# Optimization experiments

Measured on AMD Instinct MI355X. Metric: run time of the kernel, lower is better.

The kernel has to match this reference:

```python
import jax, jax.numpy as jnp
import numpy as np

DIM = 128
IND_DIM = 5
HEADS = 4
DIM_HEAD = 32
HIDDEN = HEADS * DIM_HEAD  # 128
SCALE = DIM_HEAD ** -0.5


def setup_inputs() -> dict:
    key = jax.random.key(0)
    ks = jax.random.split(key, 6)
    b, n = 1, 512
    x = jax.random.normal(ks[0], (b, DIM, n), dtype=jnp.float32)
    indicator = jax.random.normal(ks[1], (b, IND_DIM, n, n), dtype=jnp.float32)
    # conv1d kernels with kernel_size=1 are just (out, in) matrices
    w_qkv = jax.random.normal(ks[2], (HIDDEN * 3, DIM), dtype=jnp.float32) * (DIM ** -0.5)
    w_ind = jax.random.normal(ks[3], (HIDDEN * 2, IND_DIM), dtype=jnp.float32) * (IND_DIM ** -0.5)
    w_out = jax.random.normal(ks[4], (DIM, HIDDEN), dtype=jnp.float32) * (HIDDEN ** -0.5)
    b_out = jax.random.normal(ks[5], (DIM,), dtype=jnp.float32) * 0.01
    return {"x": x, "indicator": indicator, "w_qkv": w_qkv,
            "w_ind": w_ind, "w_out": w_out, "b_out": b_out}


def reference(x, indicator, w_qkv, w_ind, w_out, b_out):
    b, c, n = x.shape
    h, dh = HEADS, DIM_HEAD
    # pointwise conv = channel matmul
    qkv = jnp.einsum('oc,bcn->bon', w_qkv, x)  # (b, 3*hidden, n)
    q, k, v = jnp.split(qkv, 3, axis=1)
    q = q.reshape(b, h, dh, n)
    k = k.reshape(b, h, dh, n)
    v = v.reshape(b, h, dh, n)
    ind = jnp.einsum('oc,bcij->boij', w_ind, indicator)  # (b, 2*hidden, n, n)
    ind_q, ind_k = jnp.split(ind, 2, axis=1)
    ind_q = ind_q.reshape(b, h, dh, n, n)
    ind_k = ind_k.reshape(b, h, dh, n, n)
    qq = (q[..., :, None] + ind_q) * SCALE        # (b, h, dh, n, n)
    kk = k[..., None, :] + ind_k                   # (b, h, dh, n, n)
    sim = jnp.einsum('bhdij,bhdij->bhij', qq, kk)  # (b, h, n, n)
    attn = jax.nn.softmax(sim, axis=-1)
    out = jnp.einsum('bhij,bhdj->bhdi', attn, v)   # (b, h, dh, n)
    out = out.reshape(b, h * dh, n)
    return jnp.einsum('oc,bcn->bon', w_out, out) + b_out[None, :, None]
```

## Files before the change

kernel.cpp:

```cpp
#include <hip/hip_runtime.h>
#include <hip/hip_fp16.h>
#include <math.h>

#define N      512
#define DIMC   128
#define HEADS  4
#define DH     32
#define INDC   5
#define SCALE  0.1767766952966369f

#define QKV_ROWS 384
#define AQ_BASE  384
#define AK_BASE  404
#define TOT_ROWS 424
#define NROW_BLK (TOT_ROWS / 4)

#define MHS_F    (TOT_ROWS * N / 2)
#define WOUTT_F  (MHS_F + 64)

__global__ __launch_bounds__(256) void pre_kernel(const float* __restrict__ w_qkv,
                                                  const float* __restrict__ w_ind,
                                                  const float* __restrict__ x,
                                                  const float* __restrict__ w_out,
                                                  float* __restrict__ ws) {
    const int bx = blockIdx.x;
    const int t  = threadIdx.x;
    __half* rows  = (__half*)ws;
    float* MhS    = ws + MHS_F;
    float* w_outT = ws + WOUTT_F;

    if (bx == NROW_BLK) {
        if (blockIdx.y != 0) return;
        __shared__ float mraw[HEADS * INDC * INDC];
        if (t < HEADS * INDC * INDC) {
            const int h = t / 25, c = (t / 5) % 5, cc = t % 5;
            float acc = 0.f;
            for (int d = 0; d < DH; ++d)
                acc = fmaf(w_ind[(h * DH + d) * INDC + c],
                           w_ind[(DIMC + h * DH + d) * INDC + cc], acc);
            mraw[t] = acc;
        }
        __syncthreads();
        if (t < 64) {
            const int h = t >> 4, idx = t & 15;
            const int PC[10]  = {0, 0, 0, 0, 1, 1, 1, 2, 2, 3};
            const int PCC[10] = {1, 2, 3, 4, 2, 3, 4, 3, 4, 4};
            float s = 0.f;
            if (idx < 5) {
                s = mraw[h * 25 + idx * 5 + idx];
            } else if (idx < 15) {
                const int c = PC[idx - 5], cc = PCC[idx - 5];
                s = mraw[h * 25 + c * 5 + cc] + mraw[h * 25 + cc * 5 + c];
            }
            MhS[h * 16 + idx] = s;
        }
        for (int idx = t; idx < DIMC * DIMC; idx += 256) {
            const int o = idx >> 7, c = idx & 127;
            w_outT[c * DIMC + o] = w_out[idx];
        }
        return;
    }

    __shared__ float ws2[4 * DIMC];
    const int o0 = bx * 4;
    for (int idx = t; idx < 4 * DIMC; idx += 256) {
        const int r = idx & 3, m = idx >> 2;
        const int row = o0 + r;
        float val;
        if (row < QKV_ROWS) {
            val = w_qkv[row * DIMC + m];
        } else if (row < AK_BASE) {
            const int rr = row - AQ_BASE, h = rr / INDC, c = rr % INDC;
            float acc = 0.f;
            for (int d = 0; d < DH; ++d)
                acc = fmaf(w_qkv[(h * DH + d) * DIMC + m],
                           w_ind[(DIMC + h * DH + d) * INDC + c], acc);
            val = acc;
        } else {
            const int rr = row - AK_BASE, h = rr / INDC, c = rr % INDC;
            float acc = 0.f;
            for (int d = 0; d < DH; ++d)
                acc = fmaf(w_qkv[(DIMC + h * DH + d) * DIMC + m],
                           w_ind[(h * DH + d) * INDC + c], acc);
            val = acc;
        }
        ws2[m * 4 + r] = val;
    }
    __syncthreads();

    const int i = blockIdx.y * 256 + t;
    float acc[4] = {0.f, 0.f, 0.f, 0.f};
#pragma unroll 8
    for (int c = 0; c < DIMC; ++c) {
        const float xv = x[c * N + i];
        const float4 wv = *(const float4*)(ws2 + c * 4);
        acc[0] = fmaf(wv.x, xv, acc[0]);
        acc[1] = fmaf(wv.y, xv, acc[1]);
        acc[2] = fmaf(wv.z, xv, acc[2]);
        acc[3] = fmaf(wv.w, xv, acc[3]);
    }
#pragma unroll
    for (int r = 0; r < 4; ++r) rows[(o0 + r) * N + i] = __float2half(acc[r]);
}

__global__ __launch_bounds__(256) void attn_kernel(const float* __restrict__ ws,
                                                   const float* __restrict__ ind,
                                                   const float* __restrict__ b_out,
                                                   float* __restrict__ out) {
    const int i0   = blockIdx.x * 2;
    const int t    = threadIdx.x;
    const int lane = t & 63;
    const int wave = t >> 6;

    const __half* rows  = (const __half*)ws;
    const float* MhS    = ws + MHS_F;
    const float* w_outT = ws + WOUTT_F;

    const __half* q  = rows;
    const __half* Aq = rows + 3 * DIMC * N;

    __shared__ float qs[2][DIMC];
    __shared__ float aqs[2][HEADS * INDC];
    __shared__ float msS[HEADS * 16];
    __shared__ float ps[HEADS][2][N];
    __shared__ float red[HEADS][DH][64];
    __shared__ float red4[2][HEADS][2][4];
    __shared__ float attv[2][DIMC];
    __shared__ float outred[4][2][DIMC];

    if (t < DIMC) qs[0][t] = __half2float(q[t * N + i0]);
    else          qs[1][t - DIMC] = __half2float(q[(t - DIMC) * N + i0 + 1]);
    if (t < 2 * HEADS * INDC) {
        const int ii = t / (HEADS * INDC), r = t % (HEADS * INDC);
        aqs[ii][r] = __half2float(Aq[r * N + i0 + ii]);
    } else if (t < 2 * HEADS * INDC + 64) {
        msS[t - 2 * HEADS * INDC] = MhS[t - 2 * HEADS * INDC];
    }
    __syncthreads();

    float2 ic0[INDC], ic1[INDC];
#pragma unroll
    for (int c = 0; c < INDC; ++c) {
        ic0[c] = ((const float2*)(ind + (c * N + i0) * N))[t];
        ic1[c] = ((const float2*)(ind + (c * N + i0 + 1) * N))[t];
    }
    float2 prod0[15], prod1[15];
#pragma unroll
    for (int c = 0; c < INDC; ++c) {
        prod0[c] = make_float2(ic0[c].x * ic0[c].x, ic0[c].y * ic0[c].y);
        prod1[c] = make_float2(ic1[c].x * ic1[c].x, ic1[c].y * ic1[c].y);
    }
    {
        int p = 5;
#pragma unroll
        for (int c = 0; c < INDC; ++c)
#pragma unroll
            for (int cc = c + 1; cc < INDC; ++cc, ++p) {
                prod0[p] = make_float2(ic0[c].x * ic0[cc].x, ic0[c].y * ic0[cc].y);
                prod1[p] = make_float2(ic1[c].x * ic1[cc].x, ic1[c].y * ic1[cc].y);
            }
    }

    const __half2* k2  = (const __half2*)(rows + DIMC * N);
    const __half2* Ak2 = (const __half2*)(rows + (3 * DIMC + HEADS * INDC) * N);
    float2 sim0[HEADS], sim1[HEADS];
#pragma unroll
    for (int h = 0; h < HEADS; ++h) {
        float2 qk0 = {0.f, 0.f}, qk1 = {0.f, 0.f};
#pragma unroll
        for (int d = 0; d < DH; ++d) {
            const float2 kv = __half22float2(k2[(h * DH + d) * 256 + t]);
            const float q0 = qs[0][h * DH + d], q1 = qs[1][h * DH + d];
            qk0.x = fmaf(q0, kv.x, qk0.x); qk0.y = fmaf(q0, kv.y, qk0.y);
            qk1.x = fmaf(q1, kv.x, qk1.x); qk1.y = fmaf(q1, kv.y, qk1.y);
        }
        float2 lin0 = {0.f, 0.f}, lin1 = {0.f, 0.f};
#pragma unroll
        for (int c = 0; c < INDC; ++c) {
            const float2 akv = __half22float2(Ak2[(h * INDC + c) * 256 + t]);
            const float a0 = aqs[0][h * INDC + c], a1 = aqs[1][h * INDC + c];
            lin0.x = fmaf(a0 + akv.x, ic0[c].x, lin0.x);
            lin0.y = fmaf(a0 + akv.y, ic0[c].y, lin0.y);
            lin1.x = fmaf(a1 + akv.x, ic1[c].x, lin1.x);
            lin1.y = fmaf(a1 + akv.y, ic1[c].y, lin1.y);
        }
        float2 qd0 = {0.f, 0.f}, qd1 = {0.f, 0.f};
#pragma unroll
        for (int p = 0; p < 15; ++p) {
            const float sv = msS[h * 16 + p];
            qd0.x = fmaf(sv, prod0[p].x, qd0.x); qd0.y = fmaf(sv, prod0[p].y, qd0.y);
            qd1.x = fmaf(sv, prod1[p].x, qd1.x); qd1.y = fmaf(sv, prod1[p].y, qd1.y);
        }
        sim0[h].x = SCALE * (qk0.x + lin0.x + qd0.x);
        sim0[h].y = SCALE * (qk0.y + lin0.y + qd0.y);
        sim1[h].x = SCALE * (qk1.x + lin1.x + qd1.x);
        sim1[h].y = SCALE * (qk1.y + lin1.y + qd1.y);
    }

#pragma unroll
    for (int h = 0; h < HEADS; ++h) {
        float m0 = fmaxf(sim0[h].x, sim0[h].y);
        float m1 = fmaxf(sim1[h].x, sim1[h].y);
#pragma unroll
        for (int off = 32; off; off >>= 1) {
            m0 = fmaxf(m0, __shfl_down(m0, off, 64));
            m1 = fmaxf(m1, __shfl_down(m1, off, 64));
        }
        if (lane == 0) { red4[0][h][0][wave] = m0; red4[0][h][1][wave] = m1; }
    }
    __syncthreads();
    float2 e0[HEADS], e1[HEADS];
#pragma unroll
    for (int h = 0; h < HEADS; ++h) {
        const float m0 = fmaxf(fmaxf(red4[0][h][0][0], red4[0][h][0][1]),
                               fmaxf(red4[0][h][0][2], red4[0][h][0][3]));
        const float m1 = fmaxf(fmaxf(red4[0][h][1][0], red4[0][h][1][1]),
                               fmaxf(red4[0][h][1][2], red4[0][h][1][3]));
        e0[h].x = __expf(sim0[h].x - m0); e0[h].y = __expf(sim0[h].y - m0);
        e1[h].x = __expf(sim1[h].x - m1); e1[h].y = __expf(sim1[h].y - m1);
        float s0 = e0[h].x + e0[h].y, s1 = e1[h].x + e1[h].y;
#pragma unroll
        for (int off = 32; off; off >>= 1) {
            s0 += __shfl_down(s0, off, 64);
            s1 += __shfl_down(s1, off, 64);
        }
        if (lane == 0) { red4[1][h][0][wave] = s0; red4[1][h][1][wave] = s1; }
    }
    __syncthreads();
#pragma unroll
    for (int h = 0; h < HEADS; ++h) {
        const float s0 = (red4[1][h][0][0] + red4[1][h][0][1]) +
                         (red4[1][h][0][2] + red4[1][h][0][3]);
        const float s1 = (red4[1][h][1][0] + red4[1][h][1][1]) +
                         (red4[1][h][1][2] + red4[1][h][1][3]);
        const float r0 = 1.f / s0, r1 = 1.f / s1;
        ((float2*)&ps[h][0][0])[t] = make_float2(e0[h].x * r0, e0[h].y * r0);
        ((float2*)&ps[h][1][0])[t] = make_float2(e1[h].x * r1, e1[h].y * r1);
    }
    __syncthreads();

    {
        const int h = wave;
        float acc0[DH], acc1[DH];
#pragma unroll
        for (int d = 0; d < DH; ++d) { acc0[d] = 0.f; acc1[d] = 0.f; }
        const float2* ps0 = (const float2*)&ps[h][0][0];
        const float2* ps1 = (const float2*)&ps[h][1][0];
        const __half2* v2 = (const __half2*)(rows + 2 * DIMC * N);
        for (int s = 0; s < 4; ++s) {
            const float2 p0 = ps0[lane + 64 * s];
            const float2 p1 = ps1[lane + 64 * s];
#pragma unroll
            for (int d = 0; d < DH; ++d) {
                const float2 vv = __half22float2(v2[(h * DH + d) * 256 + lane + 64 * s]);
                acc0[d] = fmaf(p0.x, vv.x, fmaf(p0.y, vv.y, acc0[d]));
                acc1[d] = fmaf(p1.x, vv.x, fmaf(p1.y, vv.y, acc1[d]));
            }
        }
        const int d = lane & 31, half = lane >> 5;
#pragma unroll
        for (int dd = 0; dd < DH; ++dd) red[h][dd][lane ^ dd] = acc0[dd];
        float s = 0.f;
#pragma unroll
        for (int kk = 0; kk < 32; ++kk) s += red[h][d][(half * 32 + kk) ^ d];
        s += __shfl_down(s, 32, 64);
        if (lane < 32) attv[0][h * DH + d] = s;
#pragma unroll
        for (int dd = 0; dd < DH; ++dd) red[h][dd][lane ^ dd] = acc1[dd];
        s = 0.f;
#pragma unroll
        for (int kk = 0; kk < 32; ++kk) s += red[h][d][(half * 32 + kk) ^ d];
        s += __shfl_down(s, 32, 64);
        if (lane < 32) attv[1][h * DH + d] = s;
    }
    __syncthreads();

    {
        const int po = t & 63;
        const int quarter = t >> 6;
        const float2* wT2 = (const float2*)w_outT;
        float2 a0 = {0.f, 0.f}, a1 = {0.f, 0.f};
#pragma unroll 8
        for (int c = quarter * 32; c < quarter * 32 + 32; ++c) {
            const float2 wv = wT2[c * 64 + po];
            const float av0 = attv[0][c], av1 = attv[1][c];
            a0.x = fmaf(wv.x, av0, a0.x); a0.y = fmaf(wv.y, av0, a0.y);
            a1.x = fmaf(wv.x, av1, a1.x); a1.y = fmaf(wv.y, av1, a1.y);
        }
        ((float2*)&outred[quarter][0][0])[po] = a0;
        ((float2*)&outred[quarter][1][0])[po] = a1;
    }
    __syncthreads();
    {
        const int o = t & 127, ii = t >> 7;
        out[o * N + i0 + ii] = ((outred[0][ii][o] + outred[1][ii][o]) +
                                (outred[2][ii][o] + outred[3][ii][o])) + b_out[o];
    }
}

extern "C" void kernel_launch(void* const* d_in, const int* in_sizes, int n_in,
                              void* d_out, int out_size, void* d_ws, size_t ws_size,
                              hipStream_t stream) {
    const float* x         = (const float*)d_in[0];
    const float* indicator = (const float*)d_in[1];
    const float* w_qkv     = (const float*)d_in[2];
    const float* w_ind     = (const float*)d_in[3];
    const float* w_out     = (const float*)d_in[4];
    const float* b_out     = (const float*)d_in[5];
    float* out = (float*)d_out;
    float* ws  = (float*)d_ws;

    pre_kernel<<<dim3(NROW_BLK + 1, 2), 256, 0, stream>>>(w_qkv, w_ind, x, w_out, ws);
    attn_kernel<<<N / 2, 256, 0, stream>>>(ws, indicator, b_out, out);
}
```

Before: 101.4 us.

## Split attention kernel across heads and accumulate output projection with atomics

The attention kernel grid gains a head dimension, so each block handles one head for two query rows. The block count grows fourfold and the per-block register and shared-memory footprint shrinks. The output projection is split per head and summed into the output with atomicAdd, and the bias is pre-written by extra blocks in the pre-kernel. The quadratic indicator term now uses the full 5x5 matrix instead of the 15 pair products. In exchange, each of the four head blocks reloads the same indicator rows, and the atomics add contention and make the summation order nondeterministic.

```diff
diff --git a/kernel.cpp b/kernel.cpp
--- a/kernel.cpp
+++ b/kernel.cpp
@@ -16,12 +16,14 @@
 #define NROW_BLK (TOT_ROWS / 4)
 
 #define MHS_F    (TOT_ROWS * N / 2)
-#define WOUTT_F  (MHS_F + 64)
+#define WOUTT_F  (MHS_F + 128)
 
 __global__ __launch_bounds__(256) void pre_kernel(const float* __restrict__ w_qkv,
                                                   const float* __restrict__ w_ind,
                                                   const float* __restrict__ x,
                                                   const float* __restrict__ w_out,
+                                                  const float* __restrict__ b_out,
+                                                  float* __restrict__ out,
                                                   float* __restrict__ ws) {
     const int bx = blockIdx.x;
     const int t  = threadIdx.x;
@@ -29,30 +31,20 @@
     float* MhS    = ws + MHS_F;
     float* w_outT = ws + WOUTT_F;
 
+    if (bx == NROW_BLK + 1) {
+        const int i = blockIdx.y * 256 + t;
+        for (int o = 0; o < DIMC; ++o) out[o * N + i] = b_out[o];
+        return;
+    }
     if (bx == NROW_BLK) {
         if (blockIdx.y != 0) return;
-        __shared__ float mraw[HEADS * INDC * INDC];
         if (t < HEADS * INDC * INDC) {
-            const int h = t / 25, c = (t / 5) % 5, cc = t % 5;
+            const int h = t / 25, idx = t % 25, c = idx / 5, cc = idx % 5;
             float acc = 0.f;
             for (int d = 0; d < DH; ++d)
                 acc = fmaf(w_ind[(h * DH + d) * INDC + c],
                            w_ind[(DIMC + h * DH + d) * INDC + cc], acc);
-            mraw[t] = acc;
-        }
-        __syncthreads();
-        if (t < 64) {
-            const int h = t >> 4, idx = t & 15;
-            const int PC[10]  = {0, 0, 0, 0, 1, 1, 1, 2, 2, 3};
-            const int PCC[10] = {1, 2, 3, 4, 2, 3, 4, 3, 4, 4};
-            float s = 0.f;
-            if (idx < 5) {
-                s = mraw[h * 25 + idx * 5 + idx];
-            } else if (idx < 15) {
-                const int c = PC[idx - 5], cc = PCC[idx - 5];
-                s = mraw[h * 25 + c * 5 + cc] + mraw[h * 25 + cc * 5 + c];
-            }
-            MhS[h * 16 + idx] = s;
+            MhS[h * 32 + idx] = acc;
         }
         for (int idx = t; idx < DIMC * DIMC; idx += 256) {
             const int o = idx >> 7, c = idx & 127;
@@ -105,9 +97,9 @@
 
 __global__ __launch_bounds__(256) void attn_kernel(const float* __restrict__ ws,
                                                    const float* __restrict__ ind,
-                                                   const float* __restrict__ b_out,
                                                    float* __restrict__ out) {
     const int i0   = blockIdx.x * 2;
+    const int h    = blockIdx.y;
     const int t    = threadIdx.x;
     const int lane = t & 63;
     const int wave = t >> 6;
@@ -119,23 +111,21 @@
     const __half* q  = rows;
     const __half* Aq = rows + 3 * DIMC * N;
 
-    __shared__ float qs[2][DIMC];
-    __shared__ float aqs[2][HEADS * INDC];
-    __shared__ float msS[HEADS * 16];
-    __shared__ float ps[HEADS][2][N];
-    __shared__ float red[HEADS][DH][64];
-    __shared__ float red4[2][HEADS][2][4];
-    __shared__ float attv[2][DIMC];
-    __shared__ float outred[4][2][DIMC];
-
-    if (t < DIMC) qs[0][t] = __half2float(q[t * N + i0]);
-    else          qs[1][t - DIMC] = __half2float(q[(t - DIMC) * N + i0 + 1]);
-    if (t < 2 * HEADS * INDC) {
-        const int ii = t / (HEADS * INDC), r = t % (HEADS * INDC);
-        aqs[ii][r] = __half2float(Aq[r * N + i0 + ii]);
-    } else if (t < 2 * HEADS * INDC + 64) {
-        msS[t - 2 * HEADS * INDC] = MhS[t - 2 * HEADS * INDC];
-    }
+    __shared__ float qs[2][DH];
+    __shared__ float aqs[2][INDC];
+    __shared__ float ms[INDC * INDC];
+    __shared__ float ps[2][N];
+    __shared__ float red4[2][2][4];
+    __shared__ float attv[2][DH];
+
+    if (t < DH)            qs[0][t]      = __half2float(q[(h * DH + t) * N + i0]);
+    else if (t < 2 * DH)   qs[1][t - DH] = __half2float(q[(h * DH + t - DH) * N + i0 + 1]);
+    else if (t < 2 * DH + INDC)
+        aqs[0][t - 2 * DH] = __half2float(Aq[(h * INDC + t - 2 * DH) * N + i0]);
+    else if (t < 2 * DH + 2 * INDC)
+        aqs[1][t - 2 * DH - INDC] = __half2float(Aq[(h * INDC + t - 2 * DH - INDC) * N + i0 + 1]);
+    else if (t >= 96 && t < 96 + 25)
+        ms[t - 96] = MhS[h * 32 + (t - 96)];
     __syncthreads();
 
     float2 ic0[INDC], ic1[INDC];
@@ -144,157 +134,112 @@
         ic0[c] = ((const float2*)(ind + (c * N + i0) * N))[t];
         ic1[c] = ((const float2*)(ind + (c * N + i0 + 1) * N))[t];
     }
-    float2 prod0[15], prod1[15];
-#pragma unroll
-    for (int c = 0; c < INDC; ++c) {
-        prod0[c] = make_float2(ic0[c].x * ic0[c].x, ic0[c].y * ic0[c].y);
-        prod1[c] = make_float2(ic1[c].x * ic1[c].x, ic1[c].y * ic1[c].y);
-    }
-    {
-        int p = 5;
-#pragma unroll
-        for (int c = 0; c < INDC; ++c)
-#pragma unroll
-            for (int cc = c + 1; cc < INDC; ++cc, ++p) {
-                prod0[p] = make_float2(ic0[c].x * ic0[cc].x, ic0[c].y * ic0[cc].y);
-                prod1[p] = make_float2(ic1[c].x * ic1[cc].x, ic1[c].y * ic1[cc].y);
-            }
-    }
 
     const __half2* k2  = (const __half2*)(rows + DIMC * N);
     const __half2* Ak2 = (const __half2*)(rows + (3 * DIMC + HEADS * INDC) * N);
-    float2 sim0[HEADS], sim1[HEADS];
-#pragma unroll
-    for (int h = 0; h < HEADS; ++h) {
-        float2 qk0 = {0.f, 0.f}, qk1 = {0.f, 0.f};
-#pragma unroll
-        for (int d = 0; d < DH; ++d) {
-            const float2 kv = __half22float2(k2[(h * DH + d) * 256 + t]);
-            const float q0 = qs[0][h * DH + d], q1 = qs[1][h * DH + d];
-            qk0.x = fmaf(q0, kv.x, qk0.x); qk0.y = fmaf(q0, kv.y, qk0.y);
-            qk1.x = fmaf(q1, kv.x, qk1.x); qk1.y = fmaf(q1, kv.y, qk1.y);
-        }
-        float2 lin0 = {0.f, 0.f}, lin1 = {0.f, 0.f};
-#pragma unroll
-        for (int c = 0; c < INDC; ++c) {
-            const float2 akv = __half22float2(Ak2[(h * INDC + c) * 256 + t]);
-            const float a0 = aqs[0][h * INDC + c], a1 = aqs[1][h * INDC + c];
-            lin0.x = fmaf(a0 + akv.x, ic0[c].x, lin0.x);
-            lin0.y = fmaf(a0 + akv.y, ic0[c].y, lin0.y);
-            lin1.x = fmaf(a1 + akv.x, ic1[c].x, lin1.x);
-            lin1.y = fmaf(a1 + akv.y, ic1[c].y, lin1.y);
-        }
-        float2 qd0 = {0.f, 0.f}, qd1 = {0.f, 0.f};
-#pragma unroll
-        for (int p = 0; p < 15; ++p) {
-            const float sv = msS[h * 16 + p];
-            qd0.x = fmaf(sv, prod0[p].x, qd0.x); qd0.y = fmaf(sv, prod0[p].y, qd0.y);
-            qd1.x = fmaf(sv, prod1[p].x, qd1.x); qd1.y = fmaf(sv, prod1[p].y, qd1.y);
-        }
-        sim0[h].x = SCALE * (qk0.x + lin0.x + qd0.x);
-        sim0[h].y = SCALE * (qk0.y + lin0.y + qd0.y);
-        sim1[h].x = SCALE * (qk1.x + lin1.x + qd1.x);
-        sim1[h].y = SCALE * (qk1.y + lin1.y + qd1.y);
-    }
-
-#pragma unroll
-    for (int h = 0; h < HEADS; ++h) {
-        float m0 = fmaxf(sim0[h].x, sim0[h].y);
-        float m1 = fmaxf(sim1[h].x, sim1[h].y);
-#pragma unroll
-        for (int off = 32; off; off >>= 1) {
-            m0 = fmaxf(m0, __shfl_down(m0, off, 64));
-            m1 = fmaxf(m1, __shfl_down(m1, off, 64));
-        }
-        if (lane == 0) { red4[0][h][0][wave] = m0; red4[0][h][1][wave] = m1; }
-    }
-    __syncthreads();
-    float2 e0[HEADS], e1[HEADS];
-#pragma unroll
-    for (int h = 0; h < HEADS; ++h) {
-        const float m0 = fmaxf(fmaxf(red4[0][h][0][0], red4[0][h][0][1]),
-                               fmaxf(red4[0][h][0][2], red4[0][h][0][3]));
-        const float m1 = fmaxf(fmaxf(red4[0][h][1][0], red4[0][h][1][1]),
-                               fmaxf(red4[0][h][1][2], red4[0][h][1][3]));
-        e0[h].x = __expf(sim0[h].x - m0); e0[h].y = __expf(sim0[h].y - m0);
-        e1[h].x = __expf(sim1[h].x - m1); e1[h].y = __expf(sim1[h].y - m1);
-        float s0 = e0[h].x + e0[h].y, s1 = e1[h].x + e1[h].y;
-#pragma unroll
-        for (int off = 32; off; off >>= 1) {
-            s0 += __shfl_down(s0, off, 64);
-            s1 += __shfl_down(s1, off, 64);
-        }
-        if (lane == 0) { red4[1][h][0][wave] = s0; red4[1][h][1][wave] = s1; }
-    }
-    __syncthreads();
-#pragma unroll
-    for (int h = 0; h < HEADS; ++h) {
-        const float s0 = (red4[1][h][0][0] + red4[1][h][0][1]) +
-                         (red4[1][h][0][2] + red4[1][h][0][3]);
-        const float s1 = (red4[1][h][1][0] + red4[1][h][1][1]) +
-                         (red4[1][h][1][2] + red4[1][h][1][3]);
-        const float r0 = 1.f / s0, r1 = 1.f / s1;
-        ((float2*)&ps[h][0][0])[t] = make_float2(e0[h].x * r0, e0[h].y * r0);
-        ((float2*)&ps[h][1][0])[t] = make_float2(e1[h].x * r1, e1[h].y * r1);
-    }
+
+    float2 qk0 = {0.f, 0.f}, qk1 = {0.f, 0.f};
+#pragma unroll
+    for (int d = 0; d < DH; ++d) {
+        const float2 kv = __half22float2(k2[(h * DH + d) * 256 + t]);
+        const float q0 = qs[0][d], q1 = qs[1][d];
+        qk0.x = fmaf(q0, kv.x, qk0.x); qk0.y = fmaf(q0, kv.y, qk0.y);
+        qk1.x = fmaf(q1, kv.x, qk1.x); qk1.y = fmaf(q1, kv.y, qk1.y);
+    }
+    float2 lin0 = {0.f, 0.f}, lin1 = {0.f, 0.f};
+#pragma unroll
+    for (int c = 0; c < INDC; ++c) {
+        const float2 akv = __half22float2(Ak2[(h * INDC + c) * 256 + t]);
+        const float a0 = aqs[0][c], a1 = aqs[1][c];
+        lin0.x = fmaf(a0 + akv.x, ic0[c].x, lin0.x);
+        lin0.y = fmaf(a0 + akv.y, ic0[c].y, lin0.y);
+        lin1.x = fmaf(a1 + akv.x, ic1[c].x, lin1.x);
+        lin1.y = fmaf(a1 + akv.y, ic1[c].y, lin1.y);
+    }
+    float2 qd0 = {0.f, 0.f}, qd1 = {0.f, 0.f};
+#pragma unroll
+    for (int c = 0; c < INDC; ++c) {
+        float2 t0 = {0.f, 0.f}, t1 = {0.f, 0.f};
+#pragma unroll
+        for (int cc = 0; cc < INDC; ++cc) {
+            const float mv = ms[c * INDC + cc];
+            t0.x = fmaf(mv, ic0[cc].x, t0.x); t0.y = fmaf(mv, ic0[cc].y, t0.y);
+            t1.x = fmaf(mv, ic1[cc].x, t1.x); t1.y = fmaf(mv, ic1[cc].y, t1.y);
+        }
+        qd0.x = fmaf(ic0[c].x, t0.x, qd0.x); qd0.y = fmaf(ic0[c].y, t0.y, qd0.y);
+        qd1.x = fmaf(ic1[c].x, t1.x, qd1.x); qd1.y = fmaf(ic1[c].y, t1.y, qd1.y);
+    }
+    const float s0x = SCALE * (qk0.x + lin0.x + qd0.x);
+    const float s0y = SCALE * (qk0.y + lin0.y + qd0.y);
+    const float s1x = SCALE * (qk1.x + lin1.x + qd1.x);
+    const float s1y = SCALE * (qk1.y + lin1.y + qd1.y);
+
+    float m0 = fmaxf(s0x, s0y), m1 = fmaxf(s1x, s1y);
+#pragma unroll
+    for (int off = 32; off; off >>= 1) {
+        m0 = fmaxf(m0, __shfl_down(m0, off, 64));
+        m1 = fmaxf(m1, __shfl_down(m1, off, 64));
+    }
+    if (lane == 0) { red4[0][0][wave] = m0; red4[0][1][wave] = m1; }
+    __syncthreads();
+    m0 = fmaxf(fmaxf(red4[0][0][0], red4[0][0][1]), fmaxf(red4[0][0][2], red4[0][0][3]));
+    m1 = fmaxf(fmaxf(red4[0][1][0], red4[0][1][1]), fmaxf(red4[0][1][2], red4[0][1][3]));
+    const float e0x = __expf(s0x - m0), e0y = __expf(s0y - m0);
+    const float e1x = __expf(s1x - m1), e1y = __expf(s1y - m1);
+    float su0 = e0x + e0y, su1 = e1x + e1y;
+#pragma unroll
+    for (int off = 32; off; off >>= 1) {
+        su0 += __shfl_down(su0, off, 64);
+        su1 += __shfl_down(su1, off, 64);
+    }
+    __syncthreads();
+    if (lane == 0) { red4[1][0][wave] = su0; red4[1][1][wave] = su1; }
+    __syncthreads();
+    su0 = (red4[1][0][0] + red4[1][0][1]) + (red4[1][0][2] + red4[1][0][3]);
+    su1 = (red4[1][1][0] + red4[1][1][1]) + (red4[1][1][2] + red4[1][1][3]);
+    const float r0 = 1.f / su0, r1 = 1.f / su1;
+    ((float2*)&ps[0][0])[t] = make_float2(e0x * r0, e0y * r0);
+    ((float2*)&ps[1][0])[t] = make_float2(e1x * r1, e1y * r1);
     __syncthreads();
 
     {
-        const int h = wave;
-        float acc0[DH], acc1[DH];
-#pragma unroll
-        for (int d = 0; d < DH; ++d) { acc0[d] = 0.f; acc1[d] = 0.f; }
-        const float2* ps0 = (const float2*)&ps[h][0][0];
-        const float2* ps1 = (const float2*)&ps[h][1][0];
+        float acc0[8], acc1[8];
+#pragma unroll
+        for (int dd = 0; dd < 8; ++dd) { acc0[dd] = 0.f; acc1[dd] = 0.f; }
+        const float2* ps0 = (const float2*)&ps[0][0];
+        const float2* ps1 = (const float2*)&ps[1][0];
         const __half2* v2 = (const __half2*)(rows + 2 * DIMC * N);
         for (int s = 0; s < 4; ++s) {
             const float2 p0 = ps0[lane + 64 * s];
             const float2 p1 = ps1[lane + 64 * s];
 #pragma unroll
-            for (int d = 0; d < DH; ++d) {
-                const float2 vv = __half22float2(v2[(h * DH + d) * 256 + lane + 64 * s]);
-                acc0[d] = fmaf(p0.x, vv.x, fmaf(p0.y, vv.y, acc0[d]));
-                acc1[d] = fmaf(p1.x, vv.x, fmaf(p1.y, vv.y, acc1[d]));
+            for (int dd = 0; dd < 8; ++dd) {
+                const float2 vv =
+                    __half22float2(v2[(h * DH + wave * 8 + dd) * 256 + lane + 64 * s]);
+                acc0[dd] = fmaf(p0.x, vv.x, fmaf(p0.y, vv.y, acc0[dd]));
+                acc1[dd] = fmaf(p1.x, vv.x, fmaf(p1.y, vv.y, acc1[dd]));
             }
         }
-        const int d = lane & 31, half = lane >> 5;
-#pragma unroll
-        for (int dd = 0; dd < DH; ++dd) red[h][dd][lane ^ dd] = acc0[dd];
-        float s = 0.f;
-#pragma unroll
-        for (int kk = 0; kk < 32; ++kk) s += red[h][d][(half * 32 + kk) ^ d];
-        s += __shfl_down(s, 32, 64);
-        if (lane < 32) attv[0][h * DH + d] = s;
-#pragma unroll
-        for (int dd = 0; dd < DH; ++dd) red[h][dd][lane ^ dd] = acc1[dd];
-        s = 0.f;
-#pragma unroll
-        for (int kk = 0; kk < 32; ++kk) s += red[h][d][(half * 32 + kk) ^ d];
-        s += __shfl_down(s, 32, 64);
-        if (lane < 32) attv[1][h * DH + d] = s;
-    }
-    __syncthreads();
-
-    {
-        const int po = t & 63;
-        const int quarter = t >> 6;
-        const float2* wT2 = (const float2*)w_outT;
-        float2 a0 = {0.f, 0.f}, a1 = {0.f, 0.f};
-#pragma unroll 8
-        for (int c = quarter * 32; c < quarter * 32 + 32; ++c) {
-            const float2 wv = wT2[c * 64 + po];
-            const float av0 = attv[0][c], av1 = attv[1][c];
-            a0.x = fmaf(wv.x, av0, a0.x); a0.y = fmaf(wv.y, av0, a0.y);
-            a1.x = fmaf(wv.x, av1, a1.x); a1.y = fmaf(wv.y, av1, a1.y);
-        }
-        ((float2*)&outred[quarter][0][0])[po] = a0;
-        ((float2*)&outred[quarter][1][0])[po] = a1;
-    }
-    __syncthreads();
+#pragma unroll
+        for (int dd = 0; dd < 8; ++dd) {
+            float a0 = acc0[dd], a1 = acc1[dd];
+#pragma unroll
+            for (int off = 32; off; off >>= 1) {
+                a0 += __shfl_down(a0, off, 64);
+                a1 += __shfl_down(a1, off, 64);
+            }
+            if (lane == 0) { attv[0][wave * 8 + dd] = a0; attv[1][wave * 8 + dd] = a1; }
+        }
+    }
+    __syncthreads();
+
     {
         const int o = t & 127, ii = t >> 7;
-        out[o * N + i0 + ii] = ((outred[0][ii][o] + outred[1][ii][o]) +
-                                (outred[2][ii][o] + outred[3][ii][o])) + b_out[o];
+        float acc = 0.f;
+#pragma unroll 8
+        for (int cc = 0; cc < DH; ++cc)
+            acc = fmaf(w_outT[(h * DH + cc) * DIMC + o], attv[ii][cc], acc);
+        atomicAdd(&out[o * N + i0 + ii], acc);
     }
 }
 
@@ -310,6 +255,7 @@
     float* out = (float*)d_out;
     float* ws  = (float*)d_ws;
 
-    pre_kernel<<<dim3(NROW_BLK + 1, 2), 256, 0, stream>>>(w_qkv, w_ind, x, w_out, ws);
-    attn_kernel<<<N / 2, 256, 0, stream>>>(ws, indicator, b_out, out);
+    pre_kernel<<<dim3(NROW_BLK + 2, 2), 256, 0, stream>>>(w_qkv, w_ind, x, w_out,
+                                                          b_out, out, ws);
+    attn_kernel<<<dim3(N / 2, HEADS), 256, 0, stream>>>(ws, indicator, out);
 }
```

Result: slower. 107.3 us (+5.8%).
